# Kernel tuning notes

Hardware: AMD Instinct MI355X
Metric: run time of the kernel (lower is better)

Reference implementation:

```python
import jax, jax.numpy as jnp
import numpy as np

B, N, H = 4, 256, 512
P = 128  # game_physics_params


def _init(key, shape, scale=0.02):
    return jax.random.normal(key, shape, dtype=jnp.float32) * scale


def setup_inputs() -> dict:
    key = jax.random.key(0)
    ks = jax.random.split(key, 16)
    return {
        "object_features": jax.random.normal(ks[0], (B, N, H), dtype=jnp.float32),
        # physics_predictor: H -> 512 -> P
        "pp_w1": _init(ks[1], (H, 512)), "pp_b1": jnp.zeros((512,), jnp.float32),
        "pp_w2": _init(ks[2], (512, P)), "pp_b2": jnp.zeros((P,), jnp.float32),
        # collision_detector: 2H -> 256 -> 128 -> 1
        "cd_w1": _init(ks[3], (2 * H, 256)), "cd_b1": jnp.zeros((256,), jnp.float32),
        "cd_w2": _init(ks[4], (256, 128)), "cd_b2": jnp.zeros((128,), jnp.float32),
        "cd_w3": _init(ks[5], (128, 1)), "cd_b3": jnp.zeros((1,), jnp.float32),
        # velocity / force heads: H -> 3
        "vel_w": _init(ks[6], (H, 3)), "vel_b": jnp.zeros((3,), jnp.float32),
        "frc_w": _init(ks[7], (H, 3)), "frc_b": jnp.zeros((3,), jnp.float32),
    }


def reference(object_features, pp_w1, pp_b1, pp_w2, pp_b2,
              cd_w1, cd_b1, cd_w2, cd_b2, cd_w3, cd_b3,
              vel_w, vel_b, frc_w, frc_b):
    x = object_features  # [B, N, H]
    # physics predictor MLP
    p = jax.nn.relu(x @ pp_w1 + pp_b1) @ pp_w2 + pp_b2  # [B, N, P]
    mass = jax.nn.sigmoid(p[..., 0:1]) * 100.0
    friction = jax.nn.sigmoid(p[..., 1:2])
    elasticity = jax.nn.sigmoid(p[..., 2:3])
    density = jax.nn.sigmoid(p[..., 3:4]) * 10.0
    velocities = x @ vel_w + vel_b  # [B, N, 3]
    forces = x @ frc_w + frc_b      # [B, N, 3]

    # vectorized pairwise collision detection over upper-triangle pairs
    iu, ju = np.triu_indices(N, k=1)  # static index arrays, length Np = N(N-1)/2
    pairs = jnp.concatenate([x[:, iu], x[:, ju]], axis=-1)  # [B, Np, 2H]
    h = jax.nn.relu(pairs @ cd_w1 + cd_b1)
    h = jax.nn.relu(h @ cd_w2 + cd_b2)
    prob = jax.nn.sigmoid(h @ cd_w3 + cd_b3)[..., 0]  # [B, Np]
    collision_matrix = jnp.zeros((x.shape[0], N, N), dtype=x.dtype)
    collision_matrix = collision_matrix.at[:, iu, ju].set(prob).at[:, ju, iu].set(prob)

    return (mass, friction, elasticity, density, velocities, forces, collision_matrix)
```

## Files before the change

kernel.cpp:

```cpp
#include <hip/hip_runtime.h>
#include <hip/hip_bf16.h>

typedef __attribute__((ext_vector_type(8))) short bf16x8;
typedef __attribute__((ext_vector_type(4))) float f32x4;

__device__ __forceinline__ float sigmoidf_(float v) {
    return 1.0f / (1.0f + __expf(-v));
}
__device__ __forceinline__ short f2bf(float f) {
    union { __hip_bfloat16 h; short s; } cv;
    cv.h = __float2bfloat16(f);
    return cv.s;
}
__device__ __forceinline__ float bf2f(short s) {
    union { float f; unsigned u; } cv;
    cv.u = ((unsigned)(unsigned short)s) << 16;
    return cv.f;
}

__global__ __launch_bounds__(256) void convert_kernel(
    const float* __restrict__ x, const float* __restrict__ pp_w1,
    const float* __restrict__ cd_w1, const float* __restrict__ cd_w2,
    const float* __restrict__ pp_w2, const float* __restrict__ vel_w,
    const float* __restrict__ frc_w,
    __hip_bfloat16* __restrict__ xb, __hip_bfloat16* __restrict__ Wt,
    __hip_bfloat16* __restrict__ w2t, float* __restrict__ hw)
{
    __shared__ float ts[64][65];
    const int b = blockIdx.x, t = threadIdx.x;

    if (b < 256) {
        int base = b * 2048 + t * 8;
        float4 a = *(const float4*)(x + base);
        float4 c = *(const float4*)(x + base + 4);
        bf16x8 o;
        o[0] = f2bf(a.x); o[1] = f2bf(a.y); o[2] = f2bf(a.z); o[3] = f2bf(a.w);
        o[4] = f2bf(c.x); o[5] = f2bf(c.y); o[6] = f2bf(c.z); o[7] = f2bf(c.w);
        *(bf16x8*)(xb + base) = o;
        return;
    }
    if (b == 392) {
        for (int e = t; e < 5120; e += 256) {
            int h = e >> 9, k = e & 511;
            float v = (h < 4) ? pp_w2[k * 128 + h]
                    : (h < 7) ? vel_w[k * 3 + (h - 4)]
                              : frc_w[k * 3 + (h - 7)];
            hw[e] = v;
        }
        return;
    }

    const float* src; int ss, k0, n0, region;
    if (b < 320)      { int i = b - 256; src = pp_w1; ss = 512; k0 = (i >> 3) * 64; n0 = (i & 7) * 64; region = 0; }
    else if (b < 384) { int i = b - 320; src = cd_w1; ss = 256; k0 = (i >> 2) * 64; n0 = (i & 3) * 64; region = 1; }
    else              { int i = b - 384; src = cd_w2; ss = 128; k0 = (i >> 1) * 64; n0 = (i & 1) * 64; region = 2; }

    #pragma unroll
    for (int i = 0; i < 4; ++i) {
        int r = (t >> 4) + i * 16, c4 = (t & 15) * 4;
        *(float4*)&ts[r][c4] = *(const float4*)(src + (k0 + r) * ss + n0 + c4);
    }
    __syncthreads();
    #pragma unroll
    for (int i = 0; i < 4; ++i) {
        int nOut = (t >> 4) + i * 16, kc = (t & 15) * 4;
        ushort4 o;
        o.x = (unsigned short)f2bf(ts[kc + 0][nOut]);
        o.y = (unsigned short)f2bf(ts[kc + 1][nOut]);
        o.z = (unsigned short)f2bf(ts[kc + 2][nOut]);
        o.w = (unsigned short)f2bf(ts[kc + 3][nOut]);
        int gn = n0 + nOut, gk = k0 + kc;
        if (region == 0)      *(ushort4*)(Wt + gn * 512 + gk) = o;
        else if (region == 1) {
            int row = (gk < 512) ? (512 + gn) : (768 + gn);
            *(ushort4*)(Wt + row * 512 + (gk & 511)) = o;
        } else                *(ushort4*)(w2t + gn * 256 + gk) = o;
    }
}

__global__ __launch_bounds__(256) void gemm_kernel(
    const __hip_bfloat16* __restrict__ xb, const __hip_bfloat16* __restrict__ Wt,
    const float* __restrict__ pp_b1, const float* __restrict__ cd_b1,
    __hip_bfloat16* __restrict__ hidg, float* __restrict__ Ug,
    float* __restrict__ Vg)
{
    const int t = threadIdx.x;
    const int wave = t >> 6, lane = t & 63;
    const int l = lane & 15, q = lane >> 4;
    const int m0 = blockIdx.y * 32;
    const int n0 = blockIdx.x * 128 + wave * 32;

    const __hip_bfloat16* a0p = xb + (m0 + l) * 512 + q * 8;
    const __hip_bfloat16* a1p = a0p + 16 * 512;
    const __hip_bfloat16* b0p = Wt + (n0 + l) * 512 + q * 8;
    const __hip_bfloat16* b1p = b0p + 16 * 512;

    f32x4 acc00 = {}, acc01 = {}, acc10 = {}, acc11 = {};
    #pragma unroll
    for (int ks = 0; ks < 16; ++ks) {
        bf16x8 a0 = *(const bf16x8*)(a0p + ks * 32);
        bf16x8 a1 = *(const bf16x8*)(a1p + ks * 32);
        bf16x8 b0 = *(const bf16x8*)(b0p + ks * 32);
        bf16x8 b1 = *(const bf16x8*)(b1p + ks * 32);
        acc00 = __builtin_amdgcn_mfma_f32_16x16x32_bf16(a0, b0, acc00, 0, 0, 0);
        acc01 = __builtin_amdgcn_mfma_f32_16x16x32_bf16(a0, b1, acc01, 0, 0, 0);
        acc10 = __builtin_amdgcn_mfma_f32_16x16x32_bf16(a1, b0, acc10, 0, 0, 0);
        acc11 = __builtin_amdgcn_mfma_f32_16x16x32_bf16(a1, b1, acc11, 0, 0, 0);
    }

    const int c0 = n0 + l, c1 = n0 + 16 + l;
    #pragma unroll
    for (int mt = 0; mt < 2; ++mt) {
        const f32x4& A0 = mt ? acc10 : acc00;
        const f32x4& A1 = mt ? acc11 : acc01;
        if (n0 < 512) {
            float b0v = pp_b1[c0], b1v = pp_b1[c1];
            #pragma unroll
            for (int r = 0; r < 4; ++r) {
                int rg = m0 + mt * 16 + q * 4 + r;
                hidg[rg * 512 + c0] = __float2bfloat16(fmaxf(A0[r] + b0v, 0.f));
                hidg[rg * 512 + c1] = __float2bfloat16(fmaxf(A1[r] + b1v, 0.f));
            }
        } else if (n0 < 768) {
            float b0v = cd_b1[c0 - 512], b1v = cd_b1[c1 - 512];
            #pragma unroll
            for (int r = 0; r < 4; ++r) {
                int rg = m0 + mt * 16 + q * 4 + r;
                Ug[rg * 256 + (c0 - 512)] = A0[r] + b0v;
                Ug[rg * 256 + (c1 - 512)] = A1[r] + b1v;
            }
        } else {
            #pragma unroll
            for (int r = 0; r < 4; ++r) {
                int rg = m0 + mt * 16 + q * 4 + r;
                Vg[rg * 256 + (c0 - 768)] = A0[r];
                Vg[rg * 256 + (c1 - 768)] = A1[r];
            }
        }
    }
}

__global__ __launch_bounds__(256, 2) void pair_kernel(
    const float* __restrict__ Ug, const float* __restrict__ Vg,
    const __hip_bfloat16* __restrict__ w2t,
    const float* __restrict__ cd_b2, const float* __restrict__ cd_w3,
    const float* __restrict__ cd_b3, float* __restrict__ cm,
    const float* __restrict__ x, const __hip_bfloat16* __restrict__ hidg,
    const float* __restrict__ hw, const float* __restrict__ pp_b2,
    const float* __restrict__ vel_b, const float* __restrict__ frc_b,
    float* __restrict__ out)
{
    __shared__ __align__(16) __hip_bfloat16 hsH[2][8192];
    __shared__ float ps[2][64][4];

    const int t = threadIdx.x;
    const int wave = t >> 6, lane = t & 63;
    const int bx = blockIdx.x;

    if (bx >= 528) {
        #pragma unroll
        for (int rr = 0; rr < 2; ++rr) {
            const int row = (bx - 528) * 8 + wave * 2 + rr;
            const float4* xr = (const float4*)(x + row * 512);
            float4 xa = xr[lane * 2], xc = xr[lane * 2 + 1];
            bf16x8 hb = *(const bf16x8*)(hidg + row * 512 + lane * 8);
            float hf[8];
            #pragma unroll
            for (int j = 0; j < 8; ++j) hf[j] = bf2f(hb[j]);

            #pragma unroll
            for (int h = 0; h < 10; ++h) {
                const float4* wr = (const float4*)(hw + h * 512);
                float4 wa = wr[lane * 2], wc = wr[lane * 2 + 1];
                float s;
                if (h < 4) {
                    s = hf[0]*wa.x + hf[1]*wa.y + hf[2]*wa.z + hf[3]*wa.w
                      + hf[4]*wc.x + hf[5]*wc.y + hf[6]*wc.z + hf[7]*wc.w;
                } else {
                    s = xa.x*wa.x + xa.y*wa.y + xa.z*wa.z + xa.w*wa.w
                      + xc.x*wc.x + xc.y*wc.y + xc.z*wc.z + xc.w*wc.w;
                }
                s += __shfl_xor(s, 1);  s += __shfl_xor(s, 2);
                s += __shfl_xor(s, 4);  s += __shfl_xor(s, 8);
                s += __shfl_xor(s, 16); s += __shfl_xor(s, 32);
                if (lane == 0) {
                    if (h < 4) {
                        float sg = sigmoidf_(s + pp_b2[h]);
                        out[h * 1024 + row] = (h == 0) ? sg * 100.f : (h == 3) ? sg * 10.f : sg;
                    } else if (h < 7) {
                        out[4096 + row * 3 + (h - 4)] = s + vel_b[h - 4];
                    } else {
                        out[7168 + row * 3 + (h - 7)] = s + frc_b[h - 7];
                    }
                }
            }
        }
        return;
    }

    const int tp = bx;
    int ti = (int)((65.0f - sqrtf(4225.0f - 8.0f * (float)tp)) * 0.5f);
    while ((ti + 1) * (65 - (ti + 1)) / 2 <= tp) ++ti;
    while (ti * (65 - ti) / 2 > tp) --ti;
    const int tj = ti + (tp - ti * (65 - ti) / 2);
    const int i0 = ti * 8, j0 = tj * 8;

    const int l = lane & 15, q = lane >> 4;
    const int xorv = (l & 7) << 4;

    const __hip_bfloat16* wb0 = w2t + ((wave * 2 + 0) * 16 + l) * 256 + q * 8;
    const __hip_bfloat16* wb1 = wb0 + 16 * 256;
    bf16x8 w2r0[8], w2r1[8];
    #pragma unroll
    for (int ks = 0; ks < 8; ++ks) {
        w2r0[ks] = *(const bf16x8*)(wb0 + ks * 32);
        w2r1[ks] = *(const bf16x8*)(wb1 + ks * 32);
    }
    const float b2v0 = cd_b2[(wave * 2 + 0) * 16 + l];
    const float b2v1 = cd_b2[(wave * 2 + 1) * 16 + l];
    const float w3v0 = cd_w3[(wave * 2 + 0) * 16 + l];
    const float w3v1 = cd_w3[(wave * 2 + 1) * 16 + l];
    const float b3 = cd_b3[0];

    f32x4 acc[4][2];
    float4 ru0[4], ru1[4], rv0[4], rv1[4];

    auto ISSUE = [&](int u, int h) {
        const float* Ub = Ug + ((u << 8) + i0) * 256 + (h << 7);
        const float* Vb = Vg + ((u << 8) + j0) * 256 + (h << 7);
        #pragma unroll
        for (int w = 0; w < 4; ++w) {
            int idx = (w << 8) + t;
            int p = idx >> 4, c = idx & 15;
            const float* up = Ub + (p >> 3) * 256 + c * 8;
            const float* vp = Vb + (p & 7) * 256 + c * 8;
            ru0[w] = *(const float4*)up;  ru1[w] = *(const float4*)(up + 4);
            rv0[w] = *(const float4*)vp;  rv1[w] = *(const float4*)(vp + 4);
        }
    };
    auto WRITE = [&](int buf) {
        char* dst = (char*)hsH[buf];
        #pragma unroll
        for (int w = 0; w < 4; ++w) {
            int idx = (w << 8) + t;
            int p = idx >> 4, c = idx & 15;
            bf16x8 o;
            o[0] = f2bf(fmaxf(ru0[w].x + rv0[w].x, 0.f));
            o[1] = f2bf(fmaxf(ru0[w].y + rv0[w].y, 0.f));
            o[2] = f2bf(fmaxf(ru0[w].z + rv0[w].z, 0.f));
            o[3] = f2bf(fmaxf(ru0[w].w + rv0[w].w, 0.f));
            o[4] = f2bf(fmaxf(ru1[w].x + rv1[w].x, 0.f));
            o[5] = f2bf(fmaxf(ru1[w].y + rv1[w].y, 0.f));
            o[6] = f2bf(fmaxf(ru1[w].z + rv1[w].z, 0.f));
            o[7] = f2bf(fmaxf(ru1[w].w + rv1[w].w, 0.f));
            int byte = (p << 8) + (((c << 4)) ^ ((p & 7) << 4));
            *(bf16x8*)(dst + byte) = o;
        }
    };
    auto MFMAH = [&](int h, int buf) {
        const char* src = (const char*)hsH[buf];
        #pragma unroll
        for (int ks = 0; ks < 4; ++ks) {
            bf16x8 bfr0 = w2r0[h * 4 + ks];
            bf16x8 bfr1 = w2r1[h * 4 + ks];
            #pragma unroll
            for (int mt = 0; mt < 4; ++mt) {
                int byte = (mt << 12) + (l << 8) + (((ks << 6) + (q << 4)) ^ xorv);
                bf16x8 afr = *(const bf16x8*)(src + byte);
                acc[mt][0] = __builtin_amdgcn_mfma_f32_16x16x32_bf16(afr, bfr0, acc[mt][0], 0, 0, 0);
                acc[mt][1] = __builtin_amdgcn_mfma_f32_16x16x32_bf16(afr, bfr1, acc[mt][1], 0, 0, 0);
            }
        }
    };
    auto EPI = [&](int u) {
        #pragma unroll
        for (int mt = 0; mt < 4; ++mt) {
            #pragma unroll
            for (int r = 0; r < 4; ++r) {
                float g0 = fmaxf(acc[mt][0][r] + b2v0, 0.f);
                float g1 = fmaxf(acc[mt][1][r] + b2v1, 0.f);
                float s = g0 * w3v0 + g1 * w3v1;
                s += __shfl_xor(s, 1);
                s += __shfl_xor(s, 2);
                s += __shfl_xor(s, 4);
                s += __shfl_xor(s, 8);
                if (l == 0) ps[u & 1][mt * 16 + q * 4 + r][wave] = s;
            }
        }
    };
    auto FIN = [&](int u) {
        if (t < 64) {
            int p = t;
            float v = ps[u & 1][p][0] + ps[u & 1][p][1] + ps[u & 1][p][2]
                    + ps[u & 1][p][3] + b3;
            float prob = 1.0f / (1.0f + __expf(-v));
            int i = i0 + (p >> 3), j = j0 + (p & 7);
            float* base = cm + u * 65536;
            if (i < j) {
                base[i * 256 + j] = prob;
                base[j * 256 + i] = prob;
            } else if (i == j) {
                base[i * 256 + i] = 0.0f;
            }
        }
    };

    ISSUE(0, 0);
    WRITE(0);
    __syncthreads();

    #pragma unroll
    for (int s = 1; s <= 8; ++s) {
        if (s < 8) ISSUE(s >> 1, s & 1);
        const int sp = s - 1, u = sp >> 1, h = sp & 1;
        if (h == 0) {
            #pragma unroll
            for (int mt = 0; mt < 4; ++mt) {
                acc[mt][0] = (f32x4){0.f, 0.f, 0.f, 0.f};
                acc[mt][1] = (f32x4){0.f, 0.f, 0.f, 0.f};
            }
        }
        MFMAH(h, h);
        if (h == 1) EPI(u);
        if ((s & 1) && s >= 3) FIN((s - 3) >> 1);
        if (s < 8) WRITE(s & 1);
        __syncthreads();
    }
    FIN(3);
}

extern "C" void kernel_launch(void* const* d_in, const int* in_sizes, int n_in,
                              void* d_out, int out_size, void* d_ws, size_t ws_size,
                              hipStream_t stream) {
    const float* x     = (const float*)d_in[0];
    const float* pp_w1 = (const float*)d_in[1];
    const float* pp_b1 = (const float*)d_in[2];
    const float* pp_w2 = (const float*)d_in[3];
    const float* pp_b2 = (const float*)d_in[4];
    const float* cd_w1 = (const float*)d_in[5];
    const float* cd_b1 = (const float*)d_in[6];
    const float* cd_w2 = (const float*)d_in[7];
    const float* cd_b2 = (const float*)d_in[8];
    const float* cd_w3 = (const float*)d_in[9];
    const float* cd_b3 = (const float*)d_in[10];
    const float* vel_w = (const float*)d_in[11];
    const float* vel_b = (const float*)d_in[12];
    const float* frc_w = (const float*)d_in[13];
    const float* frc_b = (const float*)d_in[14];

    float* out = (float*)d_out;
    float* Ug = (float*)d_ws;
    float* Vg = Ug + 262144;
    __hip_bfloat16* xb   = (__hip_bfloat16*)(Vg + 262144);
    __hip_bfloat16* Wt   = xb + 524288;
    __hip_bfloat16* hidg = Wt + 524288;
    __hip_bfloat16* w2t  = hidg + 524288;
    float* hw = (float*)(w2t + 32768);

    convert_kernel<<<dim3(393), dim3(256), 0, stream>>>(
        x, pp_w1, cd_w1, cd_w2, pp_w2, vel_w, frc_w, xb, Wt, w2t, hw);
    gemm_kernel<<<dim3(8, 32), dim3(256), 0, stream>>>(
        xb, Wt, pp_b1, cd_b1, hidg, Ug, Vg);
    pair_kernel<<<dim3(656), dim3(256), 0, stream>>>(
        Ug, Vg, w2t, cd_b2, cd_w3, cd_b3, out + 10240,
        x, hidg, hw, pp_b2, vel_b, frc_b, out);
}
```

Before: 138.6 us.

## Stage pair-kernel U/V tiles via direct global-to-LDS loads with single bf16 buffer

Replaces register-staged global loads of the U/V projection tiles with global_load_lds DMA into double-buffered raw fp32 LDS buffers. Each stage then converts (add, relu, bf16) from LDS into a single swizzled bf16 tile before the MFMA pass, with explicit waitcnt and barrier control. The aim is to free the VGPRs that held prefetched tiles and overlap the next tile's fetch with compute. The cost is an extra LDS round trip and one more barrier per stage, plus reliance on hand-written vmcnt counts.

```diff
diff --git a/kernel.cpp b/kernel.cpp
--- a/kernel.cpp
+++ b/kernel.cpp
@@ -150,7 +150,9 @@
     const float* __restrict__ vel_b, const float* __restrict__ frc_b,
     float* __restrict__ out)
 {
-    __shared__ __align__(16) __hip_bfloat16 hsH[2][8192];
+    __shared__ __align__(16) float rawU[2][1024];
+    __shared__ __align__(16) float rawV[2][1024];
+    __shared__ __align__(16) __hip_bfloat16 hs[8192];
     __shared__ float ps[2][64][4];
 
     const int t = threadIdx.x;
@@ -208,6 +210,25 @@
     const int l = lane & 15, q = lane >> 4;
     const int xorv = (l & 7) << 4;
 
+    const int dma_row = lane & 7;
+    const int dma_c4  = (wave << 3) + (lane >> 3);
+
+    auto ISSUE = [&](int s) {
+        const int u = s >> 1, h = s & 1, buf = s & 1;
+        const float* ug = Ug + (u * 256 + i0 + dma_row) * 256 + h * 128 + dma_c4 * 4;
+        const float* vg = Vg + (u * 256 + j0 + dma_row) * 256 + h * 128 + dma_c4 * 4;
+        float* lu = &rawU[buf][wave << 8];
+        float* lv = &rawV[buf][wave << 8];
+        __builtin_amdgcn_global_load_lds(
+            (const __attribute__((address_space(1))) void*)ug,
+            (__attribute__((address_space(3))) void*)lu, 16, 0, 0);
+        __builtin_amdgcn_global_load_lds(
+            (const __attribute__((address_space(1))) void*)vg,
+            (__attribute__((address_space(3))) void*)lv, 16, 0, 0);
+    };
+
+    ISSUE(0);
+
     const __hip_bfloat16* wb0 = w2t + ((wave * 2 + 0) * 16 + l) * 256 + q * 8;
     const __hip_bfloat16* wb1 = wb0 + 16 * 256;
     bf16x8 w2r0[8], w2r1[8];
@@ -223,42 +244,38 @@
     const float b3 = cd_b3[0];
 
     f32x4 acc[4][2];
-    float4 ru0[4], ru1[4], rv0[4], rv1[4];
-
-    auto ISSUE = [&](int u, int h) {
-        const float* Ub = Ug + ((u << 8) + i0) * 256 + (h << 7);
-        const float* Vb = Vg + ((u << 8) + j0) * 256 + (h << 7);
+
+    const int p_cvt = (wave << 4) + l;
+    const int pi4 = (p_cvt >> 3) << 2;
+    const int pj4 = (p_cvt & 7) << 2;
+    const int swz_cvt = (p_cvt & 7) << 4;
+
+    auto CVT = [&](int buf) {
+        const float* RU = rawU[buf];
+        const float* RV = rawV[buf];
         #pragma unroll
-        for (int w = 0; w < 4; ++w) {
-            int idx = (w << 8) + t;
-            int p = idx >> 4, c = idx & 15;
-            const float* up = Ub + (p >> 3) * 256 + c * 8;
-            const float* vp = Vb + (p & 7) * 256 + c * 8;
-            ru0[w] = *(const float4*)up;  ru1[w] = *(const float4*)(up + 4);
-            rv0[w] = *(const float4*)vp;  rv1[w] = *(const float4*)(vp + 4);
-        }
-    };
-    auto WRITE = [&](int buf) {
-        char* dst = (char*)hsH[buf];
-        #pragma unroll
-        for (int w = 0; w < 4; ++w) {
-            int idx = (w << 8) + t;
-            int p = idx >> 4, c = idx & 15;
+        for (int i = 0; i < 4; ++i) {
+            int c = (q << 2) + i;
+            float4 u0 = *(const float4*)(RU + (c << 6) + pi4);
+            float4 u1 = *(const float4*)(RU + (c << 6) + 32 + pi4);
+            float4 v0 = *(const float4*)(RV + (c << 6) + pj4);
+            float4 v1 = *(const float4*)(RV + (c << 6) + 32 + pj4);
             bf16x8 o;
-            o[0] = f2bf(fmaxf(ru0[w].x + rv0[w].x, 0.f));
-            o[1] = f2bf(fmaxf(ru0[w].y + rv0[w].y, 0.f));
-            o[2] = f2bf(fmaxf(ru0[w].z + rv0[w].z, 0.f));
-            o[3] = f2bf(fmaxf(ru0[w].w + rv0[w].w, 0.f));
-            o[4] = f2bf(fmaxf(ru1[w].x + rv1[w].x, 0.f));
-            o[5] = f2bf(fmaxf(ru1[w].y + rv1[w].y, 0.f));
-            o[6] = f2bf(fmaxf(ru1[w].z + rv1[w].z, 0.f));
-            o[7] = f2bf(fmaxf(ru1[w].w + rv1[w].w, 0.f));
-            int byte = (p << 8) + (((c << 4)) ^ ((p & 7) << 4));
-            *(bf16x8*)(dst + byte) = o;
-        }
-    };
-    auto MFMAH = [&](int h, int buf) {
-        const char* src = (const char*)hsH[buf];
+            o[0] = f2bf(fmaxf(u0.x + v0.x, 0.f));
+            o[1] = f2bf(fmaxf(u0.y + v0.y, 0.f));
+            o[2] = f2bf(fmaxf(u0.z + v0.z, 0.f));
+            o[3] = f2bf(fmaxf(u0.w + v0.w, 0.f));
+            o[4] = f2bf(fmaxf(u1.x + v1.x, 0.f));
+            o[5] = f2bf(fmaxf(u1.y + v1.y, 0.f));
+            o[6] = f2bf(fmaxf(u1.z + v1.z, 0.f));
+            o[7] = f2bf(fmaxf(u1.w + v1.w, 0.f));
+            int byte = (p_cvt << 8) + ((c << 4) ^ swz_cvt);
+            *(bf16x8*)((char*)hs + byte) = o;
+        }
+    };
+
+    auto MFMAH = [&](int h) {
+        const char* src = (const char*)hs;
         #pragma unroll
         for (int ks = 0; ks < 4; ++ks) {
             bf16x8 bfr0 = w2r0[h * 4 + ks];
@@ -305,27 +322,33 @@
         }
     };
 
-    ISSUE(0, 0);
-    WRITE(0);
-    __syncthreads();
-
-    #pragma unroll
-    for (int s = 1; s <= 8; ++s) {
-        if (s < 8) ISSUE(s >> 1, s & 1);
-        const int sp = s - 1, u = sp >> 1, h = sp & 1;
-        if (h == 0) {
+    #pragma unroll
+    for (int s = 0; s < 8; ++s) {
+        if (s < 7) {
+            ISSUE(s + 1);
+            asm volatile("s_waitcnt vmcnt(2) lgkmcnt(0)" ::: "memory");
+        } else {
+            asm volatile("s_waitcnt vmcnt(0) lgkmcnt(0)" ::: "memory");
+        }
+        __builtin_amdgcn_s_barrier();
+        __builtin_amdgcn_sched_barrier(0);
+        if ((s & 1) == 0 && s >= 2) FIN((s - 2) >> 1);
+        if ((s & 1) == 0) {
             #pragma unroll
             for (int mt = 0; mt < 4; ++mt) {
                 acc[mt][0] = (f32x4){0.f, 0.f, 0.f, 0.f};
                 acc[mt][1] = (f32x4){0.f, 0.f, 0.f, 0.f};
             }
         }
-        MFMAH(h, h);
-        if (h == 1) EPI(u);
-        if ((s & 1) && s >= 3) FIN((s - 3) >> 1);
-        if (s < 8) WRITE(s & 1);
-        __syncthreads();
-    }
+        CVT(s & 1);
+        asm volatile("s_waitcnt lgkmcnt(0)" ::: "memory");
+        __builtin_amdgcn_s_barrier();
+        __builtin_amdgcn_sched_barrier(0);
+        MFMAH(s & 1);
+        if (s & 1) EPI(s >> 1);
+    }
+    asm volatile("s_waitcnt lgkmcnt(0)" ::: "memory");
+    __builtin_amdgcn_s_barrier();
     FIN(3);
 }
 
```

New measurement: 144.7 us. 4.4% more time.

## Store U/V projections in bf16 and stream them into LDS via async loads

Applied to the files above, without the earlier changes.

The per-object U and V projections from the first GEMM are now stored in bf16 instead of fp32, halving their footprint. In the pair kernel, each block prefetches all four batches' U/V tiles directly into LDS with global_load_lds, using a swizzled layout. It then builds the pairwise ReLU(U+V) hidden tile from LDS with explicit waitcnt/barrier staging, replacing the old register double-buffered loads. The head-output blocks also cache the small head weights in LDS. The extra bf16 rounding of U and V before the add adds some precision loss.

```diff
diff --git a/kernel.cpp b/kernel.cpp
--- a/kernel.cpp
+++ b/kernel.cpp
@@ -81,8 +81,8 @@
 __global__ __launch_bounds__(256) void gemm_kernel(
     const __hip_bfloat16* __restrict__ xb, const __hip_bfloat16* __restrict__ Wt,
     const float* __restrict__ pp_b1, const float* __restrict__ cd_b1,
-    __hip_bfloat16* __restrict__ hidg, float* __restrict__ Ug,
-    float* __restrict__ Vg)
+    __hip_bfloat16* __restrict__ hidg, __hip_bfloat16* __restrict__ Ugb,
+    __hip_bfloat16* __restrict__ Vgb)
 {
     const int t = threadIdx.x;
     const int wave = t >> 6, lane = t & 63;
@@ -126,22 +126,22 @@
             #pragma unroll
             for (int r = 0; r < 4; ++r) {
                 int rg = m0 + mt * 16 + q * 4 + r;
-                Ug[rg * 256 + (c0 - 512)] = A0[r] + b0v;
-                Ug[rg * 256 + (c1 - 512)] = A1[r] + b1v;
+                Ugb[rg * 256 + (c0 - 512)] = __float2bfloat16(A0[r] + b0v);
+                Ugb[rg * 256 + (c1 - 512)] = __float2bfloat16(A1[r] + b1v);
             }
         } else {
             #pragma unroll
             for (int r = 0; r < 4; ++r) {
                 int rg = m0 + mt * 16 + q * 4 + r;
-                Vg[rg * 256 + (c0 - 768)] = A0[r];
-                Vg[rg * 256 + (c1 - 768)] = A1[r];
+                Vgb[rg * 256 + (c0 - 768)] = __float2bfloat16(A0[r]);
+                Vgb[rg * 256 + (c1 - 768)] = __float2bfloat16(A1[r]);
             }
         }
     }
 }
 
 __global__ __launch_bounds__(256, 2) void pair_kernel(
-    const float* __restrict__ Ug, const float* __restrict__ Vg,
+    const __hip_bfloat16* __restrict__ Ugb, const __hip_bfloat16* __restrict__ Vgb,
     const __hip_bfloat16* __restrict__ w2t,
     const float* __restrict__ cd_b2, const float* __restrict__ cd_w3,
     const float* __restrict__ cd_b3, float* __restrict__ cm,
@@ -150,27 +150,41 @@
     const float* __restrict__ vel_b, const float* __restrict__ frc_b,
     float* __restrict__ out)
 {
-    __shared__ __align__(16) __hip_bfloat16 hsH[2][8192];
-    __shared__ float ps[2][64][4];
+    __shared__ __align__(16) char smem[52224];
 
     const int t = threadIdx.x;
     const int wave = t >> 6, lane = t & 63;
     const int bx = blockIdx.x;
 
     if (bx >= 528) {
+        float* hwl = (float*)smem;
+        #pragma unroll
+        for (int i = 0; i < 5; ++i) {
+            int idx = i * 256 + t;
+            ((float4*)hwl)[idx] = ((const float4*)hw)[idx];
+        }
+        __syncthreads();
+
+        const int row0 = (bx - 528) * 8 + wave * 2;
+        const float4* xr0 = (const float4*)(x + row0 * 512);
+        const float4* xr1 = (const float4*)(x + (row0 + 1) * 512);
+        float4 xa0 = xr0[lane * 2], xc0 = xr0[lane * 2 + 1];
+        float4 xa1 = xr1[lane * 2], xc1 = xr1[lane * 2 + 1];
+        bf16x8 hb0 = *(const bf16x8*)(hidg + row0 * 512 + lane * 8);
+        bf16x8 hb1 = *(const bf16x8*)(hidg + (row0 + 1) * 512 + lane * 8);
+
         #pragma unroll
         for (int rr = 0; rr < 2; ++rr) {
-            const int row = (bx - 528) * 8 + wave * 2 + rr;
-            const float4* xr = (const float4*)(x + row * 512);
-            float4 xa = xr[lane * 2], xc = xr[lane * 2 + 1];
-            bf16x8 hb = *(const bf16x8*)(hidg + row * 512 + lane * 8);
+            const int row = row0 + rr;
+            float4 xa = rr ? xa1 : xa0, xc = rr ? xc1 : xc0;
+            bf16x8 hb = rr ? hb1 : hb0;
             float hf[8];
             #pragma unroll
             for (int j = 0; j < 8; ++j) hf[j] = bf2f(hb[j]);
 
             #pragma unroll
             for (int h = 0; h < 10; ++h) {
-                const float4* wr = (const float4*)(hw + h * 512);
+                const float4* wr = (const float4*)(hwl + h * 512);
                 float4 wa = wr[lane * 2], wc = wr[lane * 2 + 1];
                 float s;
                 if (h < 4) {
@@ -198,6 +212,10 @@
         return;
     }
 
+    char* rawBB = smem;
+    char* hsB   = smem + 32768;
+    float (*ps)[64][4] = (float (*)[64][4])(smem + 32768 + 17408);
+
     const int tp = bx;
     int ti = (int)((65.0f - sqrtf(4225.0f - 8.0f * (float)tp)) * 0.5f);
     while ((ti + 1) * (65 - (ti + 1)) / 2 <= tp) ++ti;
@@ -206,7 +224,6 @@
     const int i0 = ti * 8, j0 = tj * 8;
 
     const int l = lane & 15, q = lane >> 4;
-    const int xorv = (l & 7) << 4;
 
     const __hip_bfloat16* wb0 = w2t + ((wave * 2 + 0) * 16 + l) * 256 + q * 8;
     const __hip_bfloat16* wb1 = wb0 + 16 * 256;
@@ -222,51 +239,55 @@
     const float w3v1 = cd_w3[(wave * 2 + 1) * 16 + l];
     const float b3 = cd_b3[0];
 
+    __builtin_amdgcn_sched_barrier(0);
+    {
+        const int r0 = wave * 2;
+        const int rlane = r0 + (lane >> 5);
+        const int slot = lane & 31;
+        #pragma unroll
+        for (int u = 0; u < 4; ++u) {
+            const int gk16 = slot ^ (rlane & 7);
+            const __hip_bfloat16* us = Ugb + ((u << 8) + i0 + rlane) * 256 + gk16 * 8;
+            const __hip_bfloat16* vs = Vgb + ((u << 8) + j0 + rlane) * 256 + gk16 * 8;
+            char* du = rawBB + (((u << 1) + 0) * 8 + r0) * 512;
+            char* dv = rawBB + (((u << 1) + 1) * 8 + r0) * 512;
+            __builtin_amdgcn_global_load_lds(
+                (const __attribute__((address_space(1))) void*)us,
+                (__attribute__((address_space(3))) void*)du, 16, 0, 0);
+            __builtin_amdgcn_global_load_lds(
+                (const __attribute__((address_space(1))) void*)vs,
+                (__attribute__((address_space(3))) void*)dv, 16, 0, 0);
+        }
+    }
+    __builtin_amdgcn_sched_barrier(0);
+
     f32x4 acc[4][2];
-    float4 ru0[4], ru1[4], rv0[4], rv1[4];
-
-    auto ISSUE = [&](int u, int h) {
-        const float* Ub = Ug + ((u << 8) + i0) * 256 + (h << 7);
-        const float* Vb = Vg + ((u << 8) + j0) * 256 + (h << 7);
-        #pragma unroll
-        for (int w = 0; w < 4; ++w) {
-            int idx = (w << 8) + t;
-            int p = idx >> 4, c = idx & 15;
-            const float* up = Ub + (p >> 3) * 256 + c * 8;
-            const float* vp = Vb + (p & 7) * 256 + c * 8;
-            ru0[w] = *(const float4*)up;  ru1[w] = *(const float4*)(up + 4);
-            rv0[w] = *(const float4*)vp;  rv1[w] = *(const float4*)(vp + 4);
+
+    auto CVT = [&](int u, int h) {
+        const char* RU = rawBB + ((u << 1) + 0) * 4096;
+        const char* RV = rawBB + ((u << 1) + 1) * 4096;
+        const int ur = lane >> 3, vr = lane & 7;
+        #pragma unroll
+        for (int i = 0; i < 4; ++i) {
+            const int s16 = (wave << 2) + i;
+            const int gs = (h << 4) + s16;
+            bf16x8 ub = *(const bf16x8*)(RU + ur * 512 + ((gs ^ ur) << 4));
+            bf16x8 vb = *(const bf16x8*)(RV + vr * 512 + ((gs ^ vr) << 4));
+            bf16x8 o;
+            #pragma unroll
+            for (int j = 0; j < 8; ++j)
+                o[j] = f2bf(fmaxf(bf2f(ub[j]) + bf2f(vb[j]), 0.f));
+            *(bf16x8*)(hsB + s16 * 1088 + lane * 16) = o;
         }
     };
-    auto WRITE = [&](int buf) {
-        char* dst = (char*)hsH[buf];
-        #pragma unroll
-        for (int w = 0; w < 4; ++w) {
-            int idx = (w << 8) + t;
-            int p = idx >> 4, c = idx & 15;
-            bf16x8 o;
-            o[0] = f2bf(fmaxf(ru0[w].x + rv0[w].x, 0.f));
-            o[1] = f2bf(fmaxf(ru0[w].y + rv0[w].y, 0.f));
-            o[2] = f2bf(fmaxf(ru0[w].z + rv0[w].z, 0.f));
-            o[3] = f2bf(fmaxf(ru0[w].w + rv0[w].w, 0.f));
-            o[4] = f2bf(fmaxf(ru1[w].x + rv1[w].x, 0.f));
-            o[5] = f2bf(fmaxf(ru1[w].y + rv1[w].y, 0.f));
-            o[6] = f2bf(fmaxf(ru1[w].z + rv1[w].z, 0.f));
-            o[7] = f2bf(fmaxf(ru1[w].w + rv1[w].w, 0.f));
-            int byte = (p << 8) + (((c << 4)) ^ ((p & 7) << 4));
-            *(bf16x8*)(dst + byte) = o;
-        }
-    };
-    auto MFMAH = [&](int h, int buf) {
-        const char* src = (const char*)hsH[buf];
+    auto MFMAH = [&](int h) {
         #pragma unroll
         for (int ks = 0; ks < 4; ++ks) {
             bf16x8 bfr0 = w2r0[h * 4 + ks];
             bf16x8 bfr1 = w2r1[h * 4 + ks];
             #pragma unroll
             for (int mt = 0; mt < 4; ++mt) {
-                int byte = (mt << 12) + (l << 8) + (((ks << 6) + (q << 4)) ^ xorv);
-                bf16x8 afr = *(const bf16x8*)(src + byte);
+                bf16x8 afr = *(const bf16x8*)(hsB + (ks * 4 + q) * 1088 + (mt * 16 + l) * 16);
                 acc[mt][0] = __builtin_amdgcn_mfma_f32_16x16x32_bf16(afr, bfr0, acc[mt][0], 0, 0, 0);
                 acc[mt][1] = __builtin_amdgcn_mfma_f32_16x16x32_bf16(afr, bfr1, acc[mt][1], 0, 0, 0);
             }
@@ -305,27 +326,41 @@
         }
     };
 
-    ISSUE(0, 0);
-    WRITE(0);
-    __syncthreads();
-
-    #pragma unroll
-    for (int s = 1; s <= 8; ++s) {
-        if (s < 8) ISSUE(s >> 1, s & 1);
-        const int sp = s - 1, u = sp >> 1, h = sp & 1;
-        if (h == 0) {
-            #pragma unroll
-            for (int mt = 0; mt < 4; ++mt) {
-                acc[mt][0] = (f32x4){0.f, 0.f, 0.f, 0.f};
-                acc[mt][1] = (f32x4){0.f, 0.f, 0.f, 0.f};
-            }
-        }
-        MFMAH(h, h);
-        if (h == 1) EPI(u);
-        if ((s & 1) && s >= 3) FIN((s - 3) >> 1);
-        if (s < 8) WRITE(s & 1);
-        __syncthreads();
-    }
+    #pragma unroll
+    for (int u = 0; u < 4; ++u) {
+        if (u == 0)      asm volatile("s_waitcnt vmcnt(6) lgkmcnt(0)" ::: "memory");
+        else if (u == 1) asm volatile("s_waitcnt vmcnt(4) lgkmcnt(0)" ::: "memory");
+        else if (u == 2) asm volatile("s_waitcnt vmcnt(2) lgkmcnt(0)" ::: "memory");
+        else             asm volatile("s_waitcnt vmcnt(0) lgkmcnt(0)" ::: "memory");
+        __builtin_amdgcn_s_barrier();
+        __builtin_amdgcn_sched_barrier(0);
+
+        #pragma unroll
+        for (int mt = 0; mt < 4; ++mt) {
+            acc[mt][0] = (f32x4){0.f, 0.f, 0.f, 0.f};
+            acc[mt][1] = (f32x4){0.f, 0.f, 0.f, 0.f};
+        }
+
+        CVT(u, 0);
+        if (u >= 1) FIN(u - 1);
+        asm volatile("s_waitcnt lgkmcnt(0)" ::: "memory");
+        __builtin_amdgcn_s_barrier();
+        __builtin_amdgcn_sched_barrier(0);
+
+        MFMAH(0);
+        __builtin_amdgcn_s_barrier();
+        __builtin_amdgcn_sched_barrier(0);
+
+        CVT(u, 1);
+        asm volatile("s_waitcnt lgkmcnt(0)" ::: "memory");
+        __builtin_amdgcn_s_barrier();
+        __builtin_amdgcn_sched_barrier(0);
+
+        MFMAH(1);
+        EPI(u);
+    }
+    asm volatile("s_waitcnt lgkmcnt(0)" ::: "memory");
+    __builtin_amdgcn_s_barrier();
     FIN(3);
 }
 
@@ -349,9 +384,9 @@
     const float* frc_b = (const float*)d_in[14];
 
     float* out = (float*)d_out;
-    float* Ug = (float*)d_ws;
-    float* Vg = Ug + 262144;
-    __hip_bfloat16* xb   = (__hip_bfloat16*)(Vg + 262144);
+    __hip_bfloat16* Ugb  = (__hip_bfloat16*)d_ws;
+    __hip_bfloat16* Vgb  = Ugb + 262144;
+    __hip_bfloat16* xb   = Vgb + 262144;
     __hip_bfloat16* Wt   = xb + 524288;
     __hip_bfloat16* hidg = Wt + 524288;
     __hip_bfloat16* w2t  = hidg + 524288;
@@ -360,8 +395,8 @@
     convert_kernel<<<dim3(393), dim3(256), 0, stream>>>(
         x, pp_w1, cd_w1, cd_w2, pp_w2, vel_w, frc_w, xb, Wt, w2t, hw);
     gemm_kernel<<<dim3(8, 32), dim3(256), 0, stream>>>(
-        xb, Wt, pp_b1, cd_b1, hidg, Ug, Vg);
+        xb, Wt, pp_b1, cd_b1, hidg, Ugb, Vgb);
     pair_kernel<<<dim3(656), dim3(256), 0, stream>>>(
-        Ug, Vg, w2t, cd_b2, cd_w3, cd_b3, out + 10240,
+        Ugb, Vgb, w2t, cd_b2, cd_w3, cd_b3, out + 10240,
         x, hidg, hw, pp_b2, vel_b, frc_b, out);
 }
```

After: 126.7 us, median of 2. 1.09x faster.
